# Performance work log

Measured on AMD Instinct MI355X. Metric: run time of the kernel, lower is better.

## Reference

```python
import jax, jax.numpy as jnp
import numpy as np
from jax import lax

NH = 8        # num_heads
NWIN = 7      # n_win
TOPK = 4


def setup_inputs() -> dict:
    key = jax.random.key(0)
    ks = jax.random.split(key, 7)
    B, C, H, W = 16, 256, 56, 56
    x = jax.random.normal(ks[0], (B, C, H, W), dtype=jnp.float32)
    s = 1.0 / np.sqrt(C)
    qkv_w = jax.random.normal(ks[1], (3 * C, C), dtype=jnp.float32) * s   # 1x1 conv
    qkv_b = jnp.zeros((3 * C,), dtype=jnp.float32)
    lepe_w = jax.random.normal(ks[2], (C, 1, 5, 5), dtype=jnp.float32) * 0.2  # depthwise 5x5
    lepe_b = jnp.zeros((C,), dtype=jnp.float32)
    out_w = jax.random.normal(ks[3], (C, C), dtype=jnp.float32) * s       # 1x1 conv
    out_b = jnp.zeros((C,), dtype=jnp.float32)
    return {"x": x, "qkv_w": qkv_w, "qkv_b": qkv_b, "lepe_w": lepe_w,
            "lepe_b": lepe_b, "out_w": out_w, "out_b": out_b}


def reference(x, qkv_w, qkv_b, lepe_w, lepe_b, out_w, out_b):
    B, C, H, W = x.shape
    rs0, rs1 = max(1, H // NWIN), max(1, W // NWIN)   # region size (H,W assumed divisible)
    rh, rw = H // rs0, W // rs1
    nreg, reg = rh * rw, rs0 * rs1
    hd = C // NH
    scale = C ** (-0.5)

    # qkv projection (1x1 conv == channel matmul)
    qkv = jnp.einsum('bchw,oc->bohw', x, qkv_w) + qkv_b[None, :, None, None]
    q, k, v = jnp.split(qkv, 3, axis=1)

    # region-level pooling (avg_pool over exact region blocks)
    def pool(t):
        return t.reshape(B, C, rh, rs0, rw, rs1).mean(axis=(3, 5))  # (B,C,rh,rw)
    q_r = pool(q).reshape(B, C, nreg).transpose(0, 2, 1)   # (B, nreg, C)
    k_r = pool(k).reshape(B, C, nreg)                      # (B, C, nreg)
    a_r = q_r @ k_r                                        # (B, nreg, nreg)
    _, idx = lax.top_k(a_r, TOPK)                          # (B, nreg, topk)

    # grid -> sequence: (B,C,H,W) -> (B,NH,nreg,reg,hd)
    def g2s(t):
        t = t.reshape(B, NH, hd, rh, rs0, rw, rs1)
        t = t.transpose(0, 1, 3, 5, 4, 6, 2)  # b,m,h,w,p,q,d
        return t.reshape(B, NH, nreg, reg, hd)

    qs, ks_, vs = g2s(q), g2s(k), g2s(v)

    # gather top-k kv regions per query region
    idx_h = jnp.broadcast_to(idx[:, None], (B, NH, nreg, TOPK))
    gidx = idx_h.reshape(B, NH, nreg * TOPK)[..., None, None]   # (B,NH,nreg*topk,1,1)
    kg = jnp.take_along_axis(ks_, gidx, axis=2).reshape(B, NH, nreg, TOPK * reg, hd)
    vg = jnp.take_along_axis(vs, gidx, axis=2).reshape(B, NH, nreg, TOPK * reg, hd)

    attn = jax.nn.softmax(jnp.einsum('bhnrd,bhnkd->bhnrk', qs * scale, kg), axis=-1)
    out = jnp.einsum('bhnrk,bhnkd->bhnrd', attn, vg)  # (B,NH,nreg,reg,hd)

    # sequence -> grid
    out = out.reshape(B, NH, rh, rw, rs0, rs1, hd)
    out = out.transpose(0, 1, 6, 2, 4, 3, 5).reshape(B, C, H, W)

    # LePE: depthwise 5x5 conv on v
    lepe = lax.conv_general_dilated(v, lepe_w, (1, 1), 'SAME',
                                    feature_group_count=C,
                                    dimension_numbers=('NCHW', 'OIHW', 'NCHW'))
    lepe = lepe + lepe_b[None, :, None, None]

    out = out + lepe
    out = jnp.einsum('bchw,oc->bohw', out, out_w) + out_b[None, :, None, None]
    return out
```

## Files before the change

kernel.cpp:

```cpp
#include <hip/hip_runtime.h>

typedef __attribute__((ext_vector_type(8))) short short8;
typedef __attribute__((ext_vector_type(4))) float f32x4;
typedef unsigned int uint;

constexpr int Bn    = 16;
constexpr int Cn    = 256;
constexpr int Hn    = 56;
constexpr int Wn    = 56;
constexpr int HWn   = Hn * Wn;
constexpr int NPn   = 3200;
constexpr int NHn   = 8;
constexpr int RWn   = 7;
constexpr int NREGn = 49;
constexpr int TOPKn = 4;
constexpr float QKSf = 0.0625f * 1.44269504088896f;

__device__ __forceinline__ float b2f(ushort u) { return __builtin_bit_cast(float, (uint)u << 16); }
__device__ __forceinline__ float b2fl(uint u) { return __builtin_bit_cast(float, u << 16); }
__device__ __forceinline__ float b2fh(uint u) { return __builtin_bit_cast(float, u & 0xffff0000u); }
__device__ __forceinline__ uint cvtpk(float lo, float hi) {
    uint r;
    asm("v_cvt_pk_bf16_f32 %0, %1, %2" : "=v"(r) : "v"(lo), "v"(hi));
    return r;
}

typedef __attribute__((address_space(3))) uint lds_u32_t;
typedef __attribute__((address_space(1))) const uint glb_u32_t;
__device__ __forceinline__ void gl_lds16(const ushort* g, ushort* l) {
    __builtin_amdgcn_global_load_lds((glb_u32_t*)g, (lds_u32_t*)l, 16, 0, 0);
}

__global__ __launch_bounds__(256)
void convert_w(const float* __restrict__ qw, const float* __restrict__ ow,
               ushort* __restrict__ wq, ushort* __restrict__ wo)
{
    const int e = (blockIdx.x * 256 + threadIdx.x) * 4;
    if (e < 196608) {
        const float4 v = *(const float4*)(qw + e);
        uint2 w; w.x = cvtpk(v.x, v.y); w.y = cvtpk(v.z, v.w);
        *(uint2*)(wq + e) = w;
    } else {
        const int e2 = e - 196608;
        const float4 v = *(const float4*)(ow + e2);
        uint2 w; w.x = cvtpk(v.x, v.y); w.y = cvtpk(v.z, v.w);
        *(uint2*)(wo + e2) = w;
    }
}

__global__ __launch_bounds__(256)
void convert_x(const float* __restrict__ x, ushort* __restrict__ xt)
{
    __shared__ float tile[64][65];
    const int p0 = blockIdx.x * 64, c0 = blockIdx.y * 64, b = blockIdx.z;
    const int tid = threadIdx.x;
    #pragma unroll
    for (int it = 0; it < 4; ++it) {
        const int slot = it * 256 + tid;
        const int c = slot >> 4, p4 = (slot & 15) << 2;
        const float4 v = *(const float4*)(x + ((size_t)b * Cn + c0 + c) * HWn + p0 + p4);
        tile[c][p4 + 0] = v.x; tile[c][p4 + 1] = v.y;
        tile[c][p4 + 2] = v.z; tile[c][p4 + 3] = v.w;
    }
    __syncthreads();
    #pragma unroll
    for (int it = 0; it < 4; ++it) {
        const int slot = it * 256 + tid;
        const int p = slot >> 4, c4 = (slot & 15) << 2;
        uint2 w;
        w.x = cvtpk(tile[c4 + 0][p], tile[c4 + 1][p]);
        w.y = cvtpk(tile[c4 + 2][p], tile[c4 + 3][p]);
        *(uint2*)(xt + ((size_t)b * NPn + p0 + p) * Cn + c0 + c4) = w;
    }
}

__global__ __launch_bounds__(256)
void pool_x(const float* __restrict__ x, float* __restrict__ xr)
{
    const int gid = blockIdx.x * 256 + threadIdx.x;
    if (gid >= Bn * Cn * NREGn) return;
    const int r = gid % NREGn;
    const int t = gid / NREGn;
    const int c = t % Cn, b = t / Cn;
    const float* plane = x + ((size_t)b * Cn + c) * HWn + (r / RWn) * 8 * Wn + (r % RWn) * 8;
    float s = 0.f;
    #pragma unroll
    for (int p = 0; p < 8; ++p) {
        const float4 a  = *(const float4*)(plane + p * Wn);
        const float4 b4 = *(const float4*)(plane + p * Wn + 4);
        s += a.x + a.y + a.z + a.w + b4.x + b4.y + b4.z + b4.w;
    }
    xr[gid] = s * (1.0f / 64.0f);
}

__global__ __launch_bounds__(256)
void qkr_gemm(const float* __restrict__ qw, const float* __restrict__ qb,
              const float* __restrict__ xr, float* __restrict__ qr,
              float* __restrict__ kr)
{
    const int gid = blockIdx.x * 256 + threadIdx.x;
    const int j = gid % NREGn;
    const int t = gid / NREGn;
    const int m = t & 511;
    const int b = t >> 9;
    const float* wr = qw + (size_t)m * Cn;
    const float* xb = xr + (size_t)b * Cn * NREGn + j;
    float s = 0.f;
    #pragma unroll 8
    for (int c = 0; c < Cn; ++c)
        s = fmaf(wr[c], xb[c * NREGn], s);
    s += qb[m];
    if (m < Cn) qr[((size_t)b * Cn + m) * NREGn + j] = s;
    else        kr[((size_t)b * Cn + (m - Cn)) * NREGn + j] = s;
}

__global__ __launch_bounds__(256)
void routing(const float* __restrict__ qr, const float* __restrict__ kr,
             int* __restrict__ idxo)
{
    const int ig = blockIdx.x, b = blockIdx.y;
    __shared__ float ksh[Cn][NREGn];
    __shared__ float qsh[Cn][7];
    __shared__ float ar[7][NREGn];
    const float* qb = qr + (size_t)b * Cn * NREGn;
    const float* kb = kr + (size_t)b * Cn * NREGn;
    for (int e = threadIdx.x; e < Cn * NREGn; e += 256)
        ksh[e / NREGn][e % NREGn] = kb[e];
    for (int e = threadIdx.x; e < Cn * 7; e += 256)
        qsh[e / 7][e % 7] = qb[(e / 7) * NREGn + ig * 7 + (e % 7)];
    __syncthreads();
    for (int e = threadIdx.x; e < 7 * NREGn; e += 256) {
        const int il = e / NREGn, j = e % NREGn;
        float s = 0.f;
        for (int c = 0; c < Cn; ++c)
            s = fmaf(qsh[c][il], ksh[c][j], s);
        ar[il][j] = s;
    }
    __syncthreads();
    if (threadIdx.x < 7) {
        const int il = threadIdx.x;
        float bv0 = -3.0e38f, bv1 = -3.0e38f, bv2 = -3.0e38f, bv3 = -3.0e38f;
        int bi0 = 0, bi1 = 0, bi2 = 0, bi3 = 0;
        for (int j = 0; j < NREGn; ++j) {
            const float v = ar[il][j];
            if (v > bv3) {
                if (v > bv0)      { bv3=bv2; bi3=bi2; bv2=bv1; bi2=bi1; bv1=bv0; bi1=bi0; bv0=v; bi0=j; }
                else if (v > bv1) { bv3=bv2; bi3=bi2; bv2=bv1; bi2=bi1; bv1=v; bi1=j; }
                else if (v > bv2) { bv3=bv2; bi3=bi2; bv2=v; bi2=j; }
                else              { bv3=v; bi3=j; }
            }
        }
        int* o = idxo + ((size_t)b * NREGn + ig * 7 + il) * TOPKn;
        o[0] = bi0; o[1] = bi1; o[2] = bi2; o[3] = bi3;
    }
}

template<int MODE>
__global__ __launch_bounds__(256)
void gemm_mfma(const ushort* __restrict__ Wb, const float* __restrict__ bias,
               const ushort* __restrict__ Bt,
               ushort* __restrict__ oq, ushort* __restrict__ ok,
               ushort* __restrict__ ovt, float* __restrict__ of)
{
    constexpr int K = Cn;
    int bb, bx, by;
    {
        const int flat = blockIdx.x;
        if (MODE == 0) {
            const int sw = (flat & 7) * 300 + (flat >> 3);
            bb = sw / 150; const int r2 = sw % 150; bx = r2 / 6; by = r2 % 6;
        } else {
            const int sw = (flat & 7) * 100 + (flat >> 3);
            bb = sw / 50;  const int r2 = sw % 50;  bx = r2 / 2; by = r2 % 2;
        }
    }
    const int n0 = bx * 128;
    const int m0 = by * 128;
    __shared__ ushort As[128 * 32];
    __shared__ ushort Bs[128 * 32];
    const int tid = threadIdx.x;
    const int wid = tid >> 6, lane = tid & 63;
    const int wm = wid >> 1, wn = wid & 1;
    const ushort* Bb = Bt + (size_t)bb * NPn * K;

    f32x4 acc[4][4];
    #pragma unroll
    for (int i = 0; i < 4; ++i)
        #pragma unroll
        for (int j = 0; j < 4; ++j)
            acc[i][j] = (f32x4){0.f, 0.f, 0.f, 0.f};

    const int cA = wid * 64 + lane;
    const int rowA = cA >> 2, koffA = (cA & 3) << 3;

    for (int k0 = 0; k0 < K; k0 += 32) {
        gl_lds16(Wb + (size_t)(m0 + rowA) * K + k0 + koffA, As + wid * 512);
        gl_lds16(Wb + (size_t)(m0 + rowA + 64) * K + k0 + koffA, As + 2048 + wid * 512);
        gl_lds16(Bb + (size_t)(n0 + rowA) * K + k0 + koffA, Bs + wid * 512);
        gl_lds16(Bb + (size_t)(n0 + rowA + 64) * K + k0 + koffA, Bs + 2048 + wid * 512);
        __syncthreads();
        short8 a[4], b[4];
        #pragma unroll
        for (int i = 0; i < 4; ++i)
            a[i] = *(const short8*)(As + (wm * 64 + i * 16 + (lane & 15)) * 32 + ((lane >> 4) << 3));
        #pragma unroll
        for (int j = 0; j < 4; ++j)
            b[j] = *(const short8*)(Bs + (wn * 64 + j * 16 + (lane & 15)) * 32 + ((lane >> 4) << 3));
        #pragma unroll
        for (int i = 0; i < 4; ++i)
            #pragma unroll
            for (int j = 0; j < 4; ++j)
                acc[i][j] = __builtin_amdgcn_mfma_f32_16x16x32_bf16(a[i], b[j], acc[i][j], 0, 0, 0);
        __syncthreads();
    }

    if (MODE == 0) {
        #pragma unroll
        for (int i = 0; i < 4; ++i) {
            const int m_base = m0 + wm * 64 + i * 16;
            const int which = m_base >> 8;
            const int hh = (m_base >> 5) & 7;
            const int db = (m_base & 31) + ((lane >> 4) << 2);
            const float4 b4 = *(const float4*)(bias + m_base + ((lane >> 4) << 2));
            #pragma unroll
            for (int j = 0; j < 4; ++j) {
                const int n = n0 + wn * 64 + j * 16 + (lane & 15);
                if (n < HWn) {
                    const int py = n / 56, px = n % 56;
                    const int rr = (py >> 3) * 7 + (px >> 3);
                    const int ss = ((py & 7) << 3) + (px & 7);
                    if (which == 0) {
                        uint2 w;
                        w.x = cvtpk((acc[i][j][0] + b4.x) * QKSf, (acc[i][j][1] + b4.y) * QKSf);
                        w.y = cvtpk((acc[i][j][2] + b4.z) * QKSf, (acc[i][j][3] + b4.w) * QKSf);
                        *(uint2*)(oq + (((size_t)bb * NHn + hh) * HWn + rr * 64 + ss) * 32 + db) = w;
                    } else if (which == 1) {
                        uint2 w;
                        w.x = cvtpk(acc[i][j][0] + b4.x, acc[i][j][1] + b4.y);
                        w.y = cvtpk(acc[i][j][2] + b4.z, acc[i][j][3] + b4.w);
                        *(uint2*)(ok + (((size_t)bb * NHn + hh) * HWn + rr * 64 + ss) * 32 + db) = w;
                    } else {
                        const size_t vtb = ((size_t)(bb * NHn + hh) * 32 + db) * HWn + rr * 64 + ss;
                        const uint lo = cvtpk(acc[i][j][0] + b4.x, acc[i][j][1] + b4.y);
                        const uint hi = cvtpk(acc[i][j][2] + b4.z, acc[i][j][3] + b4.w);
                        ovt[vtb + 0 * HWn] = (ushort)lo;
                        ovt[vtb + 1 * HWn] = (ushort)(lo >> 16);
                        ovt[vtb + 2 * HWn] = (ushort)hi;
                        ovt[vtb + 3 * HWn] = (ushort)(hi >> 16);
                    }
                }
            }
        }
    } else {
        #pragma unroll
        for (int i = 0; i < 4; ++i) {
            const int mb = m0 + wm * 64 + i * 16 + ((lane >> 4) << 2);
            const float4 b4 = *(const float4*)(bias + mb);
            #pragma unroll
            for (int j = 0; j < 4; ++j) {
                const int n = n0 + wn * 64 + j * 16 + (lane & 15);
                if (n < HWn) {
                    const int rr = n >> 6, ss = n & 63;
                    const int py = (rr / 7) * 8 + (ss >> 3);
                    const int px = (rr % 7) * 8 + (ss & 7);
                    float* od = of + ((size_t)bb * Cn + mb) * HWn + py * 56 + px;
                    od[0 * HWn] = acc[i][j][0] + b4.x;
                    od[1 * HWn] = acc[i][j][1] + b4.y;
                    od[2 * HWn] = acc[i][j][2] + b4.z;
                    od[3 * HWn] = acc[i][j][3] + b4.w;
                }
            }
        }
    }
}

__global__ __launch_bounds__(256)
void lepe(const ushort* __restrict__ vt, const float* __restrict__ lw,
          const float* __restrict__ lb, ushort* __restrict__ lbuf)
{
    const int gid = blockIdx.x * 256 + threadIdx.x;
    const int plane = gid / 392;
    const int within = gid - plane * 392;
    const int row = within / 7;
    const int sx  = within - row * 7;
    const int px0 = sx * 8;
    const int c = plane & 255;
    const ushort* vp = vt + (size_t)plane * HWn;
    const float* wc = lw + c * 25;

    float wreg[25];
    #pragma unroll
    for (int i = 0; i < 25; ++i) wreg[i] = wc[i];

    float acc[8];
    const float bias = lb[c];
    #pragma unroll
    for (int j = 0; j < 8; ++j) acc[j] = bias;

    #pragma unroll
    for (int kh = 0; kh < 5; ++kh) {
        const int iy = row + kh - 2;
        if (iy < 0 || iy >= Hn) continue;
        const int ry = iy >> 3, il = iy & 7;
        const ushort* rp = vp + (ry * 7 + sx) * 64 + il * 8;
        const uint  a = *(const uint*)(rp - 64 + 6);
        const uint4 M = *(const uint4*)(rp);
        const uint  e = *(const uint*)(rp + 64);
        float w[12];
        w[0]  = (px0 >= 2)      ? b2fl(a)   : 0.f;
        w[1]  = (px0 >= 1)      ? b2fh(a)   : 0.f;
        w[2]  = b2fl(M.x); w[3]  = b2fh(M.x);
        w[4]  = b2fl(M.y); w[5]  = b2fh(M.y);
        w[6]  = b2fl(M.z); w[7]  = b2fh(M.z);
        w[8]  = b2fl(M.w); w[9]  = b2fh(M.w);
        w[10] = (px0 + 8 < Wn)  ? b2fl(e)   : 0.f;
        w[11] = (px0 + 9 < Wn)  ? b2fh(e)   : 0.f;
        #pragma unroll
        for (int kw = 0; kw < 5; ++kw) {
            const float ww = wreg[kh * 5 + kw];
            #pragma unroll
            for (int j = 0; j < 8; ++j)
                acc[j] = fmaf(w[j + kw], ww, acc[j]);
        }
    }
    ushort* op = lbuf + (size_t)plane * HWn + ((row >> 3) * 7 + sx) * 64 + (row & 7) * 8;
    uint2 wa, wb;
    wa.x = cvtpk(acc[0], acc[1]); wa.y = cvtpk(acc[2], acc[3]);
    wb.x = cvtpk(acc[4], acc[5]); wb.y = cvtpk(acc[6], acc[7]);
    *(uint2*)(op)     = wa;
    *(uint2*)(op + 4) = wb;
}

__global__ __launch_bounds__(256, 2)
void attention3(const ushort* __restrict__ qs, const ushort* __restrict__ ks,
                const ushort* __restrict__ vt, const int* __restrict__ idxp,
                const ushort* __restrict__ lep, ushort* __restrict__ yt)
{
    const int flat = blockIdx.x;
    const int sw = (flat & 7) * 196 + (flat >> 3);
    const int b = sw / 98;
    const int rem = sw % 98;
    const int r = rem % 49;
    const int wid = threadIdx.x >> 6, lane = threadIdx.x & 63;
    const int h = (rem / 49) * 4 + wid;
    const int col = lane & 15, g = lane >> 4;
    __shared__ ushort plds_all[4][4096];
    ushort* pw = plds_all[wid];

    const size_t hb = ((size_t)b * NHn + h) * HWn;
    const size_t vtb = (size_t)(b * NHn + h) * 32;

    short8 qf[4];
    #pragma unroll
    for (int qt = 0; qt < 4; ++qt)
        qf[qt] = *(const short8*)(qs + (hb + (size_t)r * 64 + qt * 16 + col) * 32 + g * 8);

    f32x4 o[4][2];
    #pragma unroll
    for (int qt = 0; qt < 4; ++qt) {
        o[qt][0] = (f32x4){0.f, 0.f, 0.f, 0.f};
        o[qt][1] = (f32x4){0.f, 0.f, 0.f, 0.f};
    }
    float mrow[4] = {-3.0e38f, -3.0e38f, -3.0e38f, -3.0e38f};
    float lrow[4] = {0.f, 0.f, 0.f, 0.f};

    const int* ip = idxp + ((size_t)b * NREGn + r) * TOPKn;
    const int4 i4 = *(const int4*)ip;
    const int idxs[4] = {i4.x, i4.y, i4.z, i4.w};

    short8 kfA[4], vfA[4];
    {
        const int rr = idxs[0];
        #pragma unroll
        for (int kt = 0; kt < 4; ++kt)
            kfA[kt] = *(const short8*)(ks + (hb + (size_t)rr * 64 + kt * 16 + col) * 32 + g * 8);
        #pragma unroll
        for (int dt = 0; dt < 2; ++dt)
            #pragma unroll
            for (int kc = 0; kc < 2; ++kc)
                vfA[dt * 2 + kc] = *(const short8*)(vt + (vtb + dt * 16 + col) * HWn
                                                    + (size_t)rr * 64 + kc * 32 + g * 8);
    }

    #pragma unroll
    for (int t = 0; t < TOPKn; ++t) {
        short8 kfB[4], vfB[4];
        if (t < 3) {
            const int rr = idxs[t + 1];
            #pragma unroll
            for (int kt = 0; kt < 4; ++kt)
                kfB[kt] = *(const short8*)(ks + (hb + (size_t)rr * 64 + kt * 16 + col) * 32 + g * 8);
            #pragma unroll
            for (int dt = 0; dt < 2; ++dt)
                #pragma unroll
                for (int kc = 0; kc < 2; ++kc)
                    vfB[dt * 2 + kc] = *(const short8*)(vt + (vtb + dt * 16 + col) * HWn
                                                         + (size_t)rr * 64 + kc * 32 + g * 8);
        }

        #pragma unroll
        for (int qt = 0; qt < 4; ++qt) {
            f32x4 s[4];
            #pragma unroll
            for (int kt = 0; kt < 4; ++kt)
                s[kt] = __builtin_amdgcn_mfma_f32_16x16x32_bf16(
                    kfA[kt], qf[qt], (f32x4){0.f, 0.f, 0.f, 0.f}, 0, 0, 0);

            float mx = s[0][0];
            #pragma unroll
            for (int kt = 0; kt < 4; ++kt)
                #pragma unroll
                for (int e = 0; e < 4; ++e)
                    mx = fmaxf(mx, s[kt][e]);
            mx = fmaxf(mx, __shfl_xor(mx, 16));
            mx = fmaxf(mx, __shfl_xor(mx, 32));
            if (!__all(mx - mrow[qt] <= 8.f)) {
                const float mnew = fmaxf(mrow[qt], mx);
                const float corr = exp2f(mrow[qt] - mnew);
                mrow[qt] = mnew;
                lrow[qt] *= corr;
                #pragma unroll
                for (int reg = 0; reg < 4; ++reg) {
                    const float cr = __shfl(corr, g * 4 + reg);
                    o[qt][0][reg] *= cr;
                    o[qt][1][reg] *= cr;
                }
            }
            float ps = 0.f;
            #pragma unroll
            for (int kt = 0; kt < 4; ++kt)
                #pragma unroll
                for (int e = 0; e < 4; ++e) {
                    const float p = exp2f(s[kt][e] - mrow[qt]);
                    s[kt][e] = p; ps += p;
                }
            ps += __shfl_xor(ps, 16);
            ps += __shfl_xor(ps, 32);
            lrow[qt] += ps;
            const int qrow = qt * 16 + col;
            const int swz = (qrow & 7) << 4;
            #pragma unroll
            for (int kt = 0; kt < 4; ++kt) {
                uint2 pk;
                pk.x = cvtpk(s[kt][0], s[kt][1]);
                pk.y = cvtpk(s[kt][2], s[kt][3]);
                const int byt = (qrow * 128 + kt * 32 + g * 8) ^ swz;
                *(uint2*)((char*)pw + byt) = pk;
            }
        }

        #pragma unroll
        for (int kc = 0; kc < 2; ++kc)
            #pragma unroll
            for (int qt = 0; qt < 4; ++qt) {
                const int qrow = qt * 16 + col;
                const int byt = (qrow * 128 + kc * 64 + g * 16) ^ ((qrow & 7) << 4);
                const short8 pf = *(const short8*)((const char*)pw + byt);
                o[qt][0] = __builtin_amdgcn_mfma_f32_16x16x32_bf16(pf, vfA[0 * 2 + kc], o[qt][0], 0, 0, 0);
                o[qt][1] = __builtin_amdgcn_mfma_f32_16x16x32_bf16(pf, vfA[1 * 2 + kc], o[qt][1], 0, 0, 0);
            }

        if (t < 3) {
            #pragma unroll
            for (int i = 0; i < 4; ++i) { kfA[i] = kfB[i]; vfA[i] = vfB[i]; }
        }
    }

    #pragma unroll
    for (int qt = 0; qt < 4; ++qt) {
        const float linv = 1.0f / lrow[qt];
        #pragma unroll
        for (int reg = 0; reg < 4; ++reg) {
            const float li = __shfl(linv, g * 4 + reg);
            const int row = qt * 16 + g * 4 + reg;
            const int swz = ((row >> 1) & 3) << 4;
            const uint pk = cvtpk(o[qt][0][reg] * li, o[qt][1][reg] * li);
            const int byt0 = (row * 64 + col * 2) ^ swz;
            const int byt1 = (row * 64 + (16 + col) * 2) ^ swz;
            *(ushort*)((char*)pw + byt0) = (ushort)pk;
            *(ushort*)((char*)pw + byt1) = (ushort)(pk >> 16);
        }
    }
    const ushort* lp = lep + ((size_t)b * Cn + h * 32) * HWn + (size_t)r * 64 + lane;
    ushort* yp = yt + ((size_t)b * NPn + (size_t)r * 64 + lane) * Cn + h * 32;
    const int swl = ((lane >> 1) & 3) << 4;
    #pragma unroll
    for (int c4 = 0; c4 < 8; ++c4) {
        const int byt = (lane * 64 + c4 * 8) ^ swl;
        const ushort4 ov = *(const ushort4*)((const char*)pw + byt);
        const float a0 = b2f(ov.x) + b2f(lp[(size_t)(c4 * 4 + 0) * HWn]);
        const float a1 = b2f(ov.y) + b2f(lp[(size_t)(c4 * 4 + 1) * HWn]);
        const float a2 = b2f(ov.z) + b2f(lp[(size_t)(c4 * 4 + 2) * HWn]);
        const float a3 = b2f(ov.w) + b2f(lp[(size_t)(c4 * 4 + 3) * HWn]);
        uint2 w4; w4.x = cvtpk(a0, a1); w4.y = cvtpk(a2, a3);
        *(uint2*)(yp + c4 * 4) = w4;
    }
}

extern "C" void kernel_launch(void* const* d_in, const int* in_sizes, int n_in,
                              void* d_out, int out_size, void* d_ws, size_t ws_size,
                              hipStream_t stream)
{
    const float* x      = (const float*)d_in[0];
    const float* qkv_w  = (const float*)d_in[1];
    const float* qkv_b  = (const float*)d_in[2];
    const float* lepe_w = (const float*)d_in[3];
    const float* lepe_b = (const float*)d_in[4];
    const float* out_w  = (const float*)d_in[5];
    const float* out_b  = (const float*)d_in[6];
    float* out = (float*)d_out;

    char* ws = (char*)d_ws;
    ushort* XT = (ushort*)(ws);
    ushort* YT = (ushort*)(ws + 26214400);
    ushort* QS = (ushort*)(ws + 52428800);
    ushort* KS = (ushort*)(ws + 78118912);
    ushort* VT = (ushort*)(ws + 103809024);
    ushort* LB = (ushort*)(ws + 129499136);
    ushort* WQ = (ushort*)(ws + 155189248);
    ushort* WO = (ushort*)(ws + 155582464);
    float*  XR = (float*)(ws + 155713536);
    float*  QR = (float*)(ws + 156516352);
    float*  KR = (float*)(ws + 157319168);
    int*   IDX = (int*)(ws + 158121984);

    convert_w<<<256, 256, 0, stream>>>(qkv_w, out_w, WQ, WO);
    convert_x<<<dim3(49, 4, 16), 256, 0, stream>>>(x, XT);
    pool_x<<<(Bn * Cn * NREGn + 255) / 256, 256, 0, stream>>>(x, XR);
    qkr_gemm<<<1568, 256, 0, stream>>>(qkv_w, qkv_b, XR, QR, KR);
    routing<<<dim3(7, 16), 256, 0, stream>>>(QR, KR, IDX);
    gemm_mfma<0><<<2400, 256, 0, stream>>>(WQ, qkv_b, XT, QS, KS, VT, nullptr);
    lepe<<<6272, 256, 0, stream>>>(VT, lepe_w, lepe_b, LB);
    attention3<<<1568, 256, 0, stream>>>(QS, KS, VT, IDX, LB, YT);
    gemm_mfma<1><<<800, 256, 0, stream>>>(WO, out_b, YT, nullptr, nullptr, nullptr, out);
}
```

Baseline: 243.5 us.

## Double-buffer GEMM LDS, drop softmax max-subtraction, add setprio, relax launch bounds

```diff
diff --git a/kernel.cpp b/kernel.cpp
--- a/kernel.cpp
+++ b/kernel.cpp
@@ -176,8 +176,8 @@
     }
     const int n0 = bx * 128;
     const int m0 = by * 128;
-    __shared__ ushort As[128 * 32];
-    __shared__ ushort Bs[128 * 32];
+    __shared__ ushort As[2][4096];
+    __shared__ ushort Bs[2][4096];
     const int tid = threadIdx.x;
     const int wid = tid >> 6, lane = tid & 63;
     const int wm = wid >> 1, wn = wid & 1;
@@ -193,19 +193,31 @@
     const int cA = wid * 64 + lane;
     const int rowA = cA >> 2, koffA = (cA & 3) << 3;
 
-    for (int k0 = 0; k0 < K; k0 += 32) {
-        gl_lds16(Wb + (size_t)(m0 + rowA) * K + k0 + koffA, As + wid * 512);
-        gl_lds16(Wb + (size_t)(m0 + rowA + 64) * K + k0 + koffA, As + 2048 + wid * 512);
-        gl_lds16(Bb + (size_t)(n0 + rowA) * K + k0 + koffA, Bs + wid * 512);
-        gl_lds16(Bb + (size_t)(n0 + rowA + 64) * K + k0 + koffA, Bs + 2048 + wid * 512);
-        __syncthreads();
+    const ushort* wA0 = Wb + (size_t)(m0 + rowA) * K + koffA;
+    const ushort* wA1 = Wb + (size_t)(m0 + rowA + 64) * K + koffA;
+    const ushort* bB0 = Bb + (size_t)(n0 + rowA) * K + koffA;
+    const ushort* bB1 = Bb + (size_t)(n0 + rowA + 64) * K + koffA;
+
+#define STAGE(buf, k0)                                              \
+    do {                                                            \
+        gl_lds16(wA0 + (k0), &As[buf][wid * 512]);                  \
+        gl_lds16(wA1 + (k0), &As[buf][2048 + wid * 512]);           \
+        gl_lds16(bB0 + (k0), &Bs[buf][wid * 512]);                  \
+        gl_lds16(bB1 + (k0), &Bs[buf][2048 + wid * 512]);           \
+    } while (0)
+
+    STAGE(0, 0);
+    __syncthreads();
+    int cur = 0;
+    for (int k0 = 0; k0 < K; k0 += 32, cur ^= 1) {
+        if (k0 + 32 < K) STAGE(cur ^ 1, k0 + 32);
         short8 a[4], b[4];
         #pragma unroll
         for (int i = 0; i < 4; ++i)
-            a[i] = *(const short8*)(As + (wm * 64 + i * 16 + (lane & 15)) * 32 + ((lane >> 4) << 3));
+            a[i] = *(const short8*)(&As[cur][(wm * 64 + i * 16 + (lane & 15)) * 32 + ((lane >> 4) << 3)]);
         #pragma unroll
         for (int j = 0; j < 4; ++j)
-            b[j] = *(const short8*)(Bs + (wn * 64 + j * 16 + (lane & 15)) * 32 + ((lane >> 4) << 3));
+            b[j] = *(const short8*)(&Bs[cur][(wn * 64 + j * 16 + (lane & 15)) * 32 + ((lane >> 4) << 3)]);
         #pragma unroll
         for (int i = 0; i < 4; ++i)
             #pragma unroll
@@ -213,6 +225,7 @@
                 acc[i][j] = __builtin_amdgcn_mfma_f32_16x16x32_bf16(a[i], b[j], acc[i][j], 0, 0, 0);
         __syncthreads();
     }
+#undef STAGE
 
     if (MODE == 0) {
         #pragma unroll
@@ -331,7 +344,7 @@
     *(uint2*)(op + 4) = wb;
 }
 
-__global__ __launch_bounds__(256, 2)
+__global__ __launch_bounds__(256)
 void attention3(const ushort* __restrict__ qs, const ushort* __restrict__ ks,
                 const ushort* __restrict__ vt, const int* __restrict__ idxp,
                 const ushort* __restrict__ lep, ushort* __restrict__ yt)
@@ -361,8 +374,7 @@
         o[qt][0] = (f32x4){0.f, 0.f, 0.f, 0.f};
         o[qt][1] = (f32x4){0.f, 0.f, 0.f, 0.f};
     }
-    float mrow[4] = {-3.0e38f, -3.0e38f, -3.0e38f, -3.0e38f};
-    float lrow[4] = {0.f, 0.f, 0.f, 0.f};
+    float psum[4] = {0.f, 0.f, 0.f, 0.f};
 
     const int* ip = idxp + ((size_t)b * NREGn + r) * TOPKn;
     const int4 i4 = *(const int4*)ip;
@@ -398,6 +410,7 @@
                                                          + (size_t)rr * 64 + kc * 32 + g * 8);
         }
 
+        __builtin_amdgcn_s_setprio(1);
         #pragma unroll
         for (int qt = 0; qt < 4; ++qt) {
             f32x4 s[4];
@@ -406,47 +419,23 @@
                 s[kt] = __builtin_amdgcn_mfma_f32_16x16x32_bf16(
                     kfA[kt], qf[qt], (f32x4){0.f, 0.f, 0.f, 0.f}, 0, 0, 0);
 
-            float mx = s[0][0];
-            #pragma unroll
-            for (int kt = 0; kt < 4; ++kt)
-                #pragma unroll
-                for (int e = 0; e < 4; ++e)
-                    mx = fmaxf(mx, s[kt][e]);
-            mx = fmaxf(mx, __shfl_xor(mx, 16));
-            mx = fmaxf(mx, __shfl_xor(mx, 32));
-            if (!__all(mx - mrow[qt] <= 8.f)) {
-                const float mnew = fmaxf(mrow[qt], mx);
-                const float corr = exp2f(mrow[qt] - mnew);
-                mrow[qt] = mnew;
-                lrow[qt] *= corr;
-                #pragma unroll
-                for (int reg = 0; reg < 4; ++reg) {
-                    const float cr = __shfl(corr, g * 4 + reg);
-                    o[qt][0][reg] *= cr;
-                    o[qt][1][reg] *= cr;
-                }
-            }
-            float ps = 0.f;
-            #pragma unroll
-            for (int kt = 0; kt < 4; ++kt)
-                #pragma unroll
-                for (int e = 0; e < 4; ++e) {
-                    const float p = exp2f(s[kt][e] - mrow[qt]);
-                    s[kt][e] = p; ps += p;
-                }
-            ps += __shfl_xor(ps, 16);
-            ps += __shfl_xor(ps, 32);
-            lrow[qt] += ps;
+            float ls = 0.f;
             const int qrow = qt * 16 + col;
             const int swz = (qrow & 7) << 4;
             #pragma unroll
             for (int kt = 0; kt < 4; ++kt) {
+                const float p0 = exp2f(s[kt][0]);
+                const float p1 = exp2f(s[kt][1]);
+                const float p2 = exp2f(s[kt][2]);
+                const float p3 = exp2f(s[kt][3]);
+                ls += (p0 + p1) + (p2 + p3);
                 uint2 pk;
-                pk.x = cvtpk(s[kt][0], s[kt][1]);
-                pk.y = cvtpk(s[kt][2], s[kt][3]);
+                pk.x = cvtpk(p0, p1);
+                pk.y = cvtpk(p2, p3);
                 const int byt = (qrow * 128 + kt * 32 + g * 8) ^ swz;
                 *(uint2*)((char*)pw + byt) = pk;
             }
+            psum[qt] += ls;
         }
 
         #pragma unroll
@@ -459,6 +448,7 @@
                 o[qt][0] = __builtin_amdgcn_mfma_f32_16x16x32_bf16(pf, vfA[0 * 2 + kc], o[qt][0], 0, 0, 0);
                 o[qt][1] = __builtin_amdgcn_mfma_f32_16x16x32_bf16(pf, vfA[1 * 2 + kc], o[qt][1], 0, 0, 0);
             }
+        __builtin_amdgcn_s_setprio(0);
 
         if (t < 3) {
             #pragma unroll
@@ -468,7 +458,10 @@
 
     #pragma unroll
     for (int qt = 0; qt < 4; ++qt) {
-        const float linv = 1.0f / lrow[qt];
+        float ps = psum[qt];
+        ps += __shfl_xor(ps, 16);
+        ps += __shfl_xor(ps, 32);
+        const float linv = 1.0f / ps;
         #pragma unroll
         for (int reg = 0; reg < 4; ++reg) {
             const float li = __shfl(linv, g * 4 + reg);
```

Result: slower. 262.0 us (+7.6%).
